# Performance work log

Measured on AMD Instinct MI355X. Metric: run time of the kernel, lower is better.

Reference implementation:

```python
import jax, jax.numpy as jnp
import numpy as np

DN = ('NHWC', 'HWIO', 'NHWC')
EPS = 1e-8
BN_EPS = 1e-3
ROUT_ITERS = 3


def _bn(x, p, axis):
    # p: [4, C] rows = gamma, beta, moving_mean, moving_var (inference-mode BN)
    shp = [1] * x.ndim
    shp[axis % x.ndim] = x.shape[axis % x.ndim]
    g, b, m, v = [p[i].reshape(shp) for i in range(4)]
    return (x - m) * jax.lax.rsqrt(v + BN_EPS) * g + b


def _conv(x, w, b, stride, pad):
    return jax.lax.conv_general_dilated(x, w, (stride, stride), pad, dimension_numbers=DN) + b


def _patches(x, k, s):
    # x: [B, H, W, ...] -> [B, Ho, Wo, k*k, ...] (static k*k strided slices, no big gathers)
    Ho = (x.shape[1] - k) // s + 1
    Wo = (x.shape[2] - k) // s + 1
    sl = [x[:, i:i + s * (Ho - 1) + 1:s, j:j + s * (Wo - 1) + 1:s]
          for i in range(k) for j in range(k)]
    return jnp.stack(sl, axis=3)


def _em_routing(votes, a_in, beta_a, beta_u, iters=ROUT_ITERS):
    # votes: [..., Nin, Nout, D], a_in: [..., Nin]; Hinton matrix-capsule EM routing
    Nout = votes.shape[-2]
    R = jnp.full(votes.shape[:-1], 1.0 / Nout, votes.dtype)  # [..., Nin, Nout]
    a_ex = a_in[..., None]
    for i in range(iters):
        lam = 0.01 * (i + 1)  # inverse-temperature schedule
        Ra = R * a_ex                                             # [..., Nin, Nout]
        Rs = Ra.sum(-2) + EPS                                     # [..., Nout]
        mu = jnp.einsum('...no,...nod->...od', Ra, votes) / Rs[..., None]
        diff2 = (votes - mu[..., None, :, :]) ** 2                # [..., Nin, Nout, D]
        sig2 = jnp.einsum('...no,...nod->...od', Ra, diff2) / Rs[..., None] + EPS
        cost = (beta_u[:, None] + 0.5 * jnp.log(sig2)) * Rs[..., None]
        a_out = jax.nn.sigmoid(lam * (beta_a - cost.sum(-1)))     # [..., Nout]
        if i < iters - 1:
            logp = -0.5 * jnp.sum(diff2 / sig2[..., None, :, :]
                                  + jnp.log(2.0 * jnp.pi * sig2)[..., None, :, :], axis=-1)
            R = jax.nn.softmax(jnp.log(a_out + EPS)[..., None, :] + logp, axis=-1)
    return mu, a_out


def _convcaps(pose, a, W, beta_a, beta_u, k=3, s=2):
    # pose: [B,H,W,C,4,4], a: [B,H,W,C]; W: [k*k*C, Cout, 4, 4]
    pp = _patches(pose, k, s)                  # [B,Ho,Wo,k*k,C,4,4]
    B, Ho, Wo = pp.shape[:3]
    pp = pp.reshape(B, Ho, Wo, -1, 4, 4)       # [B,Ho,Wo,Nin,4,4]
    ap = _patches(a, k, s).reshape(B, Ho, Wo, -1)
    Cout = W.shape[1]
    votes = jnp.einsum('bhwnij,nojk->bhwnoik', pp, W).reshape(B, Ho, Wo, pp.shape[3], Cout, 16)
    mu, a_out = _em_routing(votes, ap, beta_a, beta_u)
    return mu.reshape(B, Ho, Wo, Cout, 4, 4), a_out


def reference(x, conv_w, conv_b, bn1, prim_pose_w, prim_pose_b, prim_act_w, prim_act_b,
              bn2, cc1_w, cc1_ba, cc1_bu, bn3, cc2_w, cc2_ba, cc2_bu, bn4,
              dc_w, dc_ba, dc_bu, dec_w1, dec_b1, dec_w2, dec_b2, dec_w3, dec_b3):
    h = jax.nn.relu(_conv(x, conv_w, conv_b, 2, 'SAME'))          # conv1 + relu
    h = _bn(h, bn1, -1)
    pose = _conv(h, prim_pose_w, prim_pose_b, 2, 'VALID')         # PrimaryCaps pose conv
    B, H, W, _ = pose.shape
    pose = pose.reshape(B, H, W, 32, 4, 4)
    a = jax.nn.sigmoid(_conv(h, prim_act_w, prim_act_b, 2, 'VALID'))
    pose = _bn(pose, bn2, -3)
    pose, a = _convcaps(pose, a, cc1_w, cc1_ba, cc1_bu)
    pose = _bn(pose, bn3, -3)
    pose, a = _convcaps(pose, a, cc2_w, cc2_ba, cc2_bu)
    pose = _bn(pose, bn4, -3)
    # DenseCaps: flatten spatial grid of capsules
    pflat = pose.reshape(B, -1, 4, 4)                             # [B, 1152, 4, 4]
    aflat = a.reshape(B, -1)
    votes = jnp.einsum('bnij,nojk->bnoik', pflat, dc_w).reshape(B, pflat.shape[1], dc_w.shape[1], 16)
    mu, a_out = _em_routing(votes, aflat, dc_ba, dc_bu)           # mu: [B, 32, 16]
    dec_in = mu.reshape(B, -1)                                    # [B, 512]
    h = jax.nn.relu(dec_in @ dec_w1 + dec_b1)
    h = jax.nn.relu(h @ dec_w2 + dec_b2)
    return h @ dec_w3 + dec_b3


def _bn_params(k, C):
    k1, k2, k3, k4 = jax.random.split(k, 4)
    return jnp.stack([1.0 + 0.05 * jax.random.normal(k1, (C,)),
                      0.05 * jax.random.normal(k2, (C,)),
                      0.01 * jax.random.normal(k3, (C,)),
                      1.0 + 0.1 * jax.random.uniform(k4, (C,))]).astype(jnp.float32)


def setup_inputs() -> dict:
    key = jax.random.key(0)
    ks = jax.random.split(key, 24)
    B, HW, NV = 2, 128, 8192
    n = lambda k, s, sc: (sc * jax.random.normal(k, s)).astype(jnp.float32)
    return {
        'x': n(ks[0], (B, HW, HW, 3), 1.0),
        'conv_w': n(ks[1], (11, 11, 3, 96), 0.05), 'conv_b': n(ks[2], (96,), 0.05),
        'bn1': _bn_params(ks[3], 96),
        'prim_pose_w': n(ks[4], (9, 9, 96, 32 * 16), 0.05), 'prim_pose_b': n(ks[5], (32 * 16,), 0.05),
        'prim_act_w': n(ks[6], (9, 9, 96, 32), 0.05), 'prim_act_b': n(ks[7], (32,), 0.05),
        'bn2': _bn_params(ks[8], 32),
        'cc1_w': n(ks[9], (3 * 3 * 32, 32, 4, 4), 0.1),
        'cc1_ba': n(ks[10], (32,), 0.5), 'cc1_bu': n(ks[11], (32,), 0.5),
        'bn3': _bn_params(ks[12], 32),
        'cc2_w': n(ks[13], (3 * 3 * 32, 32, 4, 4), 0.1),
        'cc2_ba': n(ks[14], (32,), 0.5), 'cc2_bu': n(ks[15], (32,), 0.5),
        'bn4': _bn_params(ks[16], 32),
        'dc_w': n(ks[17], (6 * 6 * 32, 32, 4, 4), 0.1),
        'dc_ba': n(ks[18], (32,), 0.5), 'dc_bu': n(ks[19], (32,), 0.5),
        'dec_w1': n(ks[20], (512, 512), 0.05), 'dec_b1': jnp.zeros((512,), jnp.float32),
        'dec_w2': n(ks[21], (512, 1024), 0.05), 'dec_b2': jnp.zeros((1024,), jnp.float32),
        'dec_w3': n(ks[22], (1024, NV), 0.02), 'dec_b3': jnp.zeros((NV,), jnp.float32),
    }
```

## Files before the change

kernel.cpp:

```cpp
#include <hip/hip_runtime.h>
#include <hip/hip_bf16.h>

#define EPSR 1e-8f
#define BNEPS 1e-3f
#define LOG2PI 1.8378770664093453f

typedef _Float16 f16;
typedef _Float16 f16x4 __attribute__((ext_vector_type(4)));
typedef _Float16 f16x8 __attribute__((ext_vector_type(8)));
typedef float f32x4 __attribute__((ext_vector_type(4)));

#define O_H      0
#define O_POSE2  786432
#define O_ACT2   1589248
#define O_POSE3  1639424
#define O_ACT3   1812480
#define O_POSE4  1823296
#define O_ACT4   1860160
#define O_DECIN  1862464
#define O_H1     1863488
#define O_H2     1864512
#define O_PART   1866560
#define O_BWH    1997632
#define O_BWL    4485952
#define NEED_BYTES (6974272ull * 4ull)
#define O_DSTAT  0
#define O_DCOMB  32768

template<int F16>
__global__ __launch_bounds__(256) void conv1_k(
    const float* __restrict__ x, const float* __restrict__ w,
    const float* __restrict__ bias, const float* __restrict__ bn1,
    float* __restrict__ h32, f16* __restrict__ hh, f16* __restrict__ hl)
{
  int t = blockIdx.x * 256 + threadIdx.x;
  int c = t % 96; int px = t / 96;
  int ox = px & 63; int r = px >> 6; int oy = r & 63; int b = r >> 6;
  float acc = 0.f;
  int iy0 = 2*oy - 4, ix0 = 2*ox - 4;
  for (int ky = 0; ky < 11; ++ky) {
    int iy = iy0 + ky;
    if ((unsigned)iy > 127u) continue;
    const float* xrow = x + (size_t)((b*128 + iy)*128)*3;
    const float* wrow = w + (ky*11*3)*96 + c;
    for (int kx = 0; kx < 11; ++kx) {
      int ix = ix0 + kx;
      if ((unsigned)ix > 127u) continue;
      const float* xp = xrow + ix*3;
      const float* wp = wrow + kx*3*96;
      acc = fmaf(xp[0], wp[0],   acc);
      acc = fmaf(xp[1], wp[96],  acc);
      acc = fmaf(xp[2], wp[192], acc);
    }
  }
  acc += bias[c];
  acc = fmaxf(acc, 0.f);
  float g = bn1[c], be = bn1[96+c], mm = bn1[192+c], vv = bn1[288+c];
  float val = (acc - mm) * (g * rsqrtf(vv + BNEPS)) + be;
  if (F16) {
    f16 hi = (f16)val;
    f16 lo = (f16)(val - (float)hi);
    hh[t] = hi; hl[t] = lo;
  } else {
    h32[t] = val;
  }
}

__global__ __launch_bounds__(256) void split_w_k(
    const float* __restrict__ pw, const float* __restrict__ aw,
    f16* __restrict__ bwh, f16* __restrict__ bwl)
{
  __shared__ float tile[32][33];
  const int kb = blockIdx.x * 32, nb = blockIdx.y * 32;
  const int t = threadIdx.x;
  #pragma unroll
  for (int p = 0; p < 4; ++p) {
    int k_l = p*8 + (t>>5), n_l = t & 31;
    int k = kb + k_l, n = nb + n_l;
    float v = 0.f;
    if (n < 512) v = pw[(size_t)k*512 + n];
    else if (n < 544) v = aw[(size_t)k*32 + (n - 512)];
    tile[k_l][n_l] = v;
  }
  __syncthreads();
  #pragma unroll
  for (int p = 0; p < 4; ++p) {
    int n_l = p*8 + (t>>5), k_l = t & 31;
    float v = tile[k_l][n_l];
    f16 hi = (f16)v;
    f16 lo = (f16)(v - (float)hi);
    size_t dst = (size_t)(nb + n_l)*7776 + kb + k_l;
    bwh[dst] = hi; bwl[dst] = lo;
  }
}

__global__ __launch_bounds__(256) void zero_raw(float* __restrict__ pose2, float* __restrict__ act2)
{
  int t = blockIdx.x * 256 + threadIdx.x;
  if (t < 802816) pose2[t] = 0.f;
  else act2[t - 802816] = 0.f;
}

__global__ __launch_bounds__(256, 2) void conv2_mfma(
    const f16* __restrict__ hh, const f16* __restrict__ hl,
    const f16* __restrict__ bwh, const f16* __restrict__ bwl,
    float* __restrict__ pose2r, float* __restrict__ act2r)
{
  __shared__ f16 Ah[128*32];
  __shared__ f16 Al[128*32];
  __shared__ f16 Bh[128*32];
  __shared__ f16 Bl[128*32];
  const int tid = threadIdx.x;
  const int mb = blockIdx.x, nb = blockIdx.y, z = blockIdx.z;
  const int m0 = mb*128, n0 = nb*128;
  const int q = 243 / 8, rch = 243 % 8;
  const int k0 = z*q + (z < rch ? z : rch);
  const int k1 = k0 + q + (z < rch ? 1 : 0);

  const int srow = tid >> 3;
  const int c    = tid & 7;
  int habase[4]; bool amok[4];
  #pragma unroll
  for (int p = 0; p < 4; ++p) {
    int m = m0 + p*32 + srow;
    amok[p] = m < 1568;
    int mm = amok[p] ? m : 0;
    int b = mm / 784; int yx = mm - b*784; int oy = yx / 28, ox = yx - oy*28;
    habase[p] = ((b*64 + 2*oy)*64 + 2*ox)*96;
  }
  size_t bbase[4];
  #pragma unroll
  for (int p = 0; p < 4; ++p) bbase[p] = (size_t)(n0 + p*32 + srow) * 7776;

  f16x4 rah[4], ral[4], rbh[4], rbl[4];
  const f16x4 zv = {(f16)0, (f16)0, (f16)0, (f16)0};

  auto load_step = [&](int kt) {
    int ky = kt / 27, rr = kt % 27; int kx = rr / 3, ci0 = (rr % 3) * 32;
    int aoff = (ky*64 + kx)*96 + ci0 + c*4;
    int koff = kt*32 + c*4;
    #pragma unroll
    for (int p = 0; p < 4; ++p) {
      if (amok[p]) {
        rah[p] = *(const f16x4*)(hh + habase[p] + aoff);
        ral[p] = *(const f16x4*)(hl + habase[p] + aoff);
      } else { rah[p] = zv; ral[p] = zv; }
      rbh[p] = *(const f16x4*)(bwh + bbase[p] + koff);
      rbl[p] = *(const f16x4*)(bwl + bbase[p] + koff);
    }
  };

  int widx[4];
  #pragma unroll
  for (int p = 0; p < 4; ++p) {
    int row = p*32 + srow;
    widx[p] = row*32 + ((((c>>1) + (row>>1)) & 3) << 3) + ((c & 1) << 2);
  }

  const int wv = tid >> 6, lane = tid & 63;
  const int wr = wv >> 1, wc = wv & 1;
  const int l15 = lane & 15, g = lane >> 4;

  f32x4 acc[4][4];
  #pragma unroll
  for (int i = 0; i < 4; ++i)
    #pragma unroll
    for (int j = 0; j < 4; ++j) acc[i][j] = (f32x4){0.f, 0.f, 0.f, 0.f};

  int aidx[4], bidx[4];
  #pragma unroll
  for (int i = 0; i < 4; ++i) {
    int arow = wr*64 + i*16 + l15;
    aidx[i] = arow*32 + (((g + (arow>>1)) & 3) << 3);
    int brow = wc*64 + i*16 + l15;
    bidx[i] = brow*32 + (((g + (brow>>1)) & 3) << 3);
  }

  load_step(k0);
  for (int kt = k0; kt < k1; ++kt) {
    __syncthreads();
    #pragma unroll
    for (int p = 0; p < 4; ++p) {
      *(f16x4*)&Ah[widx[p]] = rah[p];
      *(f16x4*)&Al[widx[p]] = ral[p];
      *(f16x4*)&Bh[widx[p]] = rbh[p];
      *(f16x4*)&Bl[widx[p]] = rbl[p];
    }
    __syncthreads();
    if (kt + 1 < k1) load_step(kt + 1);
    f16x8 ah[4], al[4], bh[4], bl[4];
    #pragma unroll
    for (int i = 0; i < 4; ++i) {
      ah[i] = *(const f16x8*)&Ah[aidx[i]];
      al[i] = *(const f16x8*)&Al[aidx[i]];
      bh[i] = *(const f16x8*)&Bh[bidx[i]];
      bl[i] = *(const f16x8*)&Bl[bidx[i]];
    }
    #pragma unroll
    for (int i = 0; i < 4; ++i)
      #pragma unroll
      for (int j = 0; j < 4; ++j) {
        acc[i][j] = __builtin_amdgcn_mfma_f32_16x16x32_f16(ah[i], bh[j], acc[i][j], 0, 0, 0);
        acc[i][j] = __builtin_amdgcn_mfma_f32_16x16x32_f16(ah[i], bl[j], acc[i][j], 0, 0, 0);
        acc[i][j] = __builtin_amdgcn_mfma_f32_16x16x32_f16(al[i], bh[j], acc[i][j], 0, 0, 0);
      }
  }

  #pragma unroll
  for (int i = 0; i < 4; ++i) {
    #pragma unroll
    for (int j = 0; j < 4; ++j) {
      #pragma unroll
      for (int r2 = 0; r2 < 4; ++r2) {
        int m = m0 + wr*64 + i*16 + g*4 + r2;
        int n = n0 + wc*64 + j*16 + l15;
        if (m < 1568) {
          float val = acc[i][j][r2];
          if (n < 512) atomicAdd(&pose2r[(size_t)m*512 + n], val);
          else if (n < 544) atomicAdd(&act2r[(size_t)m*32 + (n - 512)], val);
        }
      }
    }
  }
}

__global__ __launch_bounds__(256) void conv2_gemm_ks(
    const float* __restrict__ h,
    const float* __restrict__ pw, const float* __restrict__ aw,
    float* __restrict__ pose2r, float* __restrict__ act2r)
{
  __shared__ float As[2][16][68];
  __shared__ float Bs[2][16][68];
  const int tid = threadIdx.x;
  const int mb = blockIdx.x, nb = blockIdx.y, z = blockIdx.z;
  const int m0 = mb * 64;
  const float* Bp; int ldB, n0;
  if (nb < 8) { Bp = pw; ldB = 512; n0 = nb * 64; } else { Bp = aw; ldB = 32; n0 = 0; }

  const int a_ml = tid & 63, a_cig = tid >> 6;
  const int am = m0 + a_ml;
  const bool am_ok = am < 1568;
  int ab_ = am / 784; int ayx = am - ab_*784;
  int aoy = ayx / 28, aox = ayx - aoy*28;
  if (!am_ok) { ab_ = 0; aoy = 0; aox = 0; }
  const float* a_base = h + (size_t)((ab_*64 + 2*aoy)*64 + 2*aox)*96 + a_cig*4;

  const int b_kk = tid >> 4, b_ng = tid & 15;
  const int b_col = b_ng * 4;
  const bool b_ok = b_col < ldB;

  const int tm = (tid & 15) * 4, tn = (tid >> 4) * 4;
  float acc[4][4] = {{0}};

  auto kidx = [](int kt, int& ky, int& kx, int& ci0) {
    int cig = kt % 6; int r = kt / 6; kx = r % 9; ky = r / 9; ci0 = cig * 16;
  };
  auto ldAv = [&](int ky, int kx, int ci0) -> float4 {
    if (!am_ok) return make_float4(0,0,0,0);
    return *(const float4*)(a_base + (ky*64 + kx)*96 + ci0);
  };
  auto ldBv = [&](int kt) -> float4 {
    if (!b_ok) return make_float4(0,0,0,0);
    return *(const float4*)(Bp + (size_t)(kt*16 + b_kk) * ldB + n0 + b_col);
  };
  auto wrAv = [&](float4 v, int buf) {
    As[buf][a_cig*4+0][a_ml] = v.x;
    As[buf][a_cig*4+1][a_ml] = v.y;
    As[buf][a_cig*4+2][a_ml] = v.z;
    As[buf][a_cig*4+3][a_ml] = v.w;
  };
  auto wrBv = [&](float4 v, int buf) {
    *(float4*)&Bs[buf][b_kk][b_col] = v;
  };

  const int kt0 = z * 81;
  {
    int ky, kx, ci0; kidx(kt0, ky, kx, ci0);
    wrAv(ldAv(ky, kx, ci0), 0); wrBv(ldBv(kt0), 0);
  }
  __syncthreads();

  for (int i = 0; i < 81; ++i) {
    int cur = i & 1;
    bool st = i < 80;
    float4 va, vb;
    if (st) {
      int ky, kx, ci0; kidx(kt0 + i + 1, ky, kx, ci0);
      va = ldAv(ky, kx, ci0);
      vb = ldBv(kt0 + i + 1);
    }
    #pragma unroll
    for (int kk = 0; kk < 16; ++kk) {
      float4 av = *(const float4*)&As[cur][kk][tm];
      float4 bv = *(const float4*)&Bs[cur][kk][tn];
      float aa[4] = {av.x, av.y, av.z, av.w};
      float bb4[4] = {bv.x, bv.y, bv.z, bv.w};
      #pragma unroll
      for (int ii = 0; ii < 4; ++ii)
        #pragma unroll
        for (int jj = 0; jj < 4; ++jj)
          acc[ii][jj] = fmaf(aa[ii], bb4[jj], acc[ii][jj]);
    }
    if (st) { wrAv(va, cur ^ 1); wrBv(vb, cur ^ 1); }
    __syncthreads();
  }

  #pragma unroll
  for (int i = 0; i < 4; ++i) {
    int m = m0 + tm + i;
    if (m >= 1568) break;
    #pragma unroll
    for (int j = 0; j < 4; ++j) {
      int nl = tn + j;
      if (nb < 8) {
        atomicAdd(&pose2r[(size_t)m*512 + n0 + nl], acc[i][j]);
      } else if (nl < 32) {
        atomicAdd(&act2r[(size_t)m*32 + nl], acc[i][j]);
      }
    }
  }
}

__global__ __launch_bounds__(256) void conv2_epi(
    const float* __restrict__ pb, const float* __restrict__ ab,
    const float* __restrict__ bn2,
    float* __restrict__ pose2, float* __restrict__ act2)
{
  int t = blockIdx.x * 256 + threadIdx.x;
  if (t < 802816) {
    int n = t & 511;
    float val = pose2[t] + pb[n];
    int caps = n >> 4;
    float g = bn2[caps], be = bn2[32+caps], mm = bn2[64+caps], vv = bn2[96+caps];
    pose2[t] = (val - mm) * (g * rsqrtf(vv + BNEPS)) + be;
  } else {
    int t2 = t - 802816;
    int nl = t2 & 31;
    float val = act2[t2] + ab[nl];
    act2[t2] = 1.f / (1.f + expf(-val));
  }
}

template<int NIN, int NWAVES, bool CONV>
__global__ __launch_bounds__(NWAVES*64) void routing_k(
    const float* __restrict__ pose_in, const float* __restrict__ act_in,
    const float* __restrict__ Wv,
    const float* __restrict__ ba, const float* __restrict__ bu,
    const float* __restrict__ bn,
    float* __restrict__ pose_out, float* __restrict__ act_out,
    int Hin, int Win, int Wout)
{
  constexpr int NT  = NWAVES * 64;
  constexpr int NPW = NIN / NWAVES;
  __shared__ float s1s[NWAVES][32*17];
  __shared__ float s2s[NWAVES][32*17];
  __shared__ float rsP[NWAVES][32];
  __shared__ float muS[32*17], isgS[32*17], lgS[32*17];
  __shared__ float laS[32], lsS[32], aoS[32], RsS[32], S0S[32];

  const int tid = threadIdx.x;
  const int wv = tid >> 6, lane = tid & 63;
  const int o = lane & 31, half = lane >> 5;

  int bb = 0, oy = 0, ox = 0;
  if (CONV) {
    int px = blockIdx.x;
    ox = px % Wout; int t2 = px / Wout; oy = t2 % Wout; bb = t2 / Wout;
  } else {
    bb = blockIdx.x;
  }

  auto ld_n = [&](int n, float4& W0, float4& W1, float4& W2, float4& W3,
                  float4& P0, float4& P1, float& AN) {
    const float* wp = Wv + (size_t)(n*32 + o) * 16;
    W0 = *(const float4*)(wp);
    W1 = *(const float4*)(wp + 4);
    W2 = *(const float4*)(wp + 8);
    W3 = *(const float4*)(wp + 12);
    const float* pp;
    if (CONV) {
      int cc = n & 31, kk = n >> 5;
      int ki = kk / 3, kj = kk - ki*3;
      int pix = (bb*Hin + 2*oy + ki)*Win + 2*ox + kj;
      pp = pose_in + (size_t)(pix*32 + cc) * 16;
      AN = act_in[pix*32 + cc];
    } else {
      pp = pose_in + (size_t)(bb*NIN + n) * 16;
      AN = act_in[bb*NIN + n];
    }
    P0 = *(const float4*)(pp + half*8);
    P1 = *(const float4*)(pp + half*8 + 4);
  };

  float mur[8], isgr[8], lar = 0.f, lsr = 0.f;
  #pragma unroll
  for (int i = 0; i < 8; ++i) { mur[i] = 0.f; isgr[i] = 0.f; }

  for (int p = 0; p < 3; ++p) {
    float lam = 0.01f * (float)(p + 1);
    float s1r[8] = {0,0,0,0,0,0,0,0};
    float s2r[8] = {0,0,0,0,0,0,0,0};
    float rsr = 0.f;

    float4 w0, w1, w2, w3, p0, p1; float an;
    ld_n(wv*NPW, w0, w1, w2, w3, p0, p1, an);

    for (int it = 0; it < NPW; ++it) {
      float4 cw0=w0, cw1=w1, cw2=w2, cw3=w3, cp0=p0, cp1=p1; float can=an;
      if (it + 1 < NPW) ld_n(wv*NPW + it + 1, w0, w1, w2, w3, p0, p1, an);

      float v[8];
      v[0] = fmaf(cp0.x,cw0.x, fmaf(cp0.y,cw1.x, fmaf(cp0.z,cw2.x, cp0.w*cw3.x)));
      v[1] = fmaf(cp0.x,cw0.y, fmaf(cp0.y,cw1.y, fmaf(cp0.z,cw2.y, cp0.w*cw3.y)));
      v[2] = fmaf(cp0.x,cw0.z, fmaf(cp0.y,cw1.z, fmaf(cp0.z,cw2.z, cp0.w*cw3.z)));
      v[3] = fmaf(cp0.x,cw0.w, fmaf(cp0.y,cw1.w, fmaf(cp0.z,cw2.w, cp0.w*cw3.w)));
      v[4] = fmaf(cp1.x,cw0.x, fmaf(cp1.y,cw1.x, fmaf(cp1.z,cw2.x, cp1.w*cw3.x)));
      v[5] = fmaf(cp1.x,cw0.y, fmaf(cp1.y,cw1.y, fmaf(cp1.z,cw2.y, cp1.w*cw3.y)));
      v[6] = fmaf(cp1.x,cw0.z, fmaf(cp1.y,cw1.z, fmaf(cp1.z,cw2.z, cp1.w*cw3.z)));
      v[7] = fmaf(cp1.x,cw0.w, fmaf(cp1.y,cw1.w, fmaf(cp1.z,cw2.w, cp1.w*cw3.w)));

      float R;
      if (p == 0) {
        R = 1.f / 32.f;
      } else {
        float t = 0.f;
        #pragma unroll
        for (int dd = 0; dd < 8; ++dd) { float df = v[dd] - mur[dd]; t = fmaf(df*df, isgr[dd], t); }
        t += __shfl_xor(t, 32, 64);
        float logit = lar - 0.5f * (t + lsr);
        float mx = logit;
        mx = fmaxf(mx, __shfl_xor(mx, 16, 64));
        mx = fmaxf(mx, __shfl_xor(mx,  8, 64));
        mx = fmaxf(mx, __shfl_xor(mx,  4, 64));
        mx = fmaxf(mx, __shfl_xor(mx,  2, 64));
        mx = fmaxf(mx, __shfl_xor(mx,  1, 64));
        float e = expf(logit - mx);
        float se = e;
        se += __shfl_xor(se, 16, 64);
        se += __shfl_xor(se,  8, 64);
        se += __shfl_xor(se,  4, 64);
        se += __shfl_xor(se,  2, 64);
        se += __shfl_xor(se,  1, 64);
        R = e / se;
      }
      float Ra = R * can;
      rsr += Ra;
      #pragma unroll
      for (int dd = 0; dd < 8; ++dd) {
        s1r[dd] = fmaf(Ra, v[dd], s1r[dd]);
        s2r[dd] = fmaf(Ra * v[dd], v[dd], s2r[dd]);
      }
    }

    #pragma unroll
    for (int dd = 0; dd < 8; ++dd) {
      s1s[wv][o*17 + half*8 + dd] = s1r[dd];
      s2s[wv][o*17 + half*8 + dd] = s2r[dd];
    }
    if (!half) rsP[wv][o] = rsr;
    __syncthreads();
    if (tid < 32) {
      float r = 0.f;
      #pragma unroll
      for (int w2 = 0; w2 < NWAVES; ++w2) r += rsP[w2][tid];
      S0S[tid] = r; RsS[tid] = r + EPSR;
    }
    __syncthreads();
    for (int idx = tid; idx < 512; idx += NT) {
      int oo = idx >> 4, d = idx & 15;
      float S1 = 0.f, S2 = 0.f;
      #pragma unroll
      for (int w2 = 0; w2 < NWAVES; ++w2) { S1 += s1s[w2][oo*17+d]; S2 += s2s[w2][oo*17+d]; }
      float Rs = RsS[oo];
      float m_ = S1 / Rs;
      float sg = (S2 - 2.f*m_*S1 + m_*m_*S0S[oo]) / Rs + EPSR;
      muS[oo*17+d]  = m_;
      isgS[oo*17+d] = 1.f / sg;
      lgS[oo*17+d]  = logf(sg);
    }
    __syncthreads();
    if (tid < 32) {
      float L = 0.f;
      #pragma unroll
      for (int d = 0; d < 16; ++d) L += lgS[tid*17 + d];
      float cost = (16.f*bu[tid] + 0.5f*L) * RsS[tid];
      float av = 1.f / (1.f + expf(-lam * (ba[tid] - cost)));
      aoS[tid] = av;
      laS[tid] = logf(av + EPSR);
      lsS[tid] = 16.f*LOG2PI + L;
    }
    __syncthreads();
    if (p < 2) {
      #pragma unroll
      for (int dd = 0; dd < 8; ++dd) {
        mur[dd]  = muS[o*17 + half*8 + dd];
        isgr[dd] = isgS[o*17 + half*8 + dd];
      }
      lar = laS[o]; lsr = lsS[o];
    }
  }

  if (CONV) {
    int pxo = (bb*Wout + oy)*Wout + ox;
    for (int idx = tid; idx < 512; idx += NT) {
      int oo = idx >> 4, d = idx & 15;
      float val = muS[oo*17 + d];
      float g = bn[oo], be = bn[32+oo], mm = bn[64+oo], vv = bn[96+oo];
      val = (val - mm) * (g * rsqrtf(vv + BNEPS)) + be;
      pose_out[(size_t)pxo*512 + idx] = val;
    }
    if (tid < 32) act_out[(size_t)pxo*32 + tid] = aoS[tid];
  } else {
    for (int idx = tid; idx < 512; idx += NT)
      pose_out[(size_t)bb*512 + idx] = muS[(idx>>4)*17 + (idx&15)];
  }
}

template<int P>
__global__ __launch_bounds__(256) void dense_stats(
    const float* __restrict__ pose_in, const float* __restrict__ act_in,
    const float* __restrict__ Wv, const float* __restrict__ comb,
    float* __restrict__ stat)
{
  __shared__ float s1s[4][32*17];
  __shared__ float s2s[4][32*17];
  __shared__ float rsP[4][32];
  const int tid = threadIdx.x;
  const int wv = tid >> 6, lane = tid & 63;
  const int o = lane & 31, half = lane >> 5;
  const int bb = blockIdx.x / 12, chunk = blockIdx.x % 12;

  float mur[8], isgr[8], lar = 0.f, lsr = 0.f;
  if (P > 0) {
    const float* cb = comb + (size_t)bb * 1088;
    #pragma unroll
    for (int dd = 0; dd < 8; ++dd) {
      mur[dd]  = cb[o*16 + half*8 + dd];
      isgr[dd] = cb[512 + o*16 + half*8 + dd];
    }
    lar = cb[1024 + o]; lsr = cb[1056 + o];
  }

  auto ld_n = [&](int n, float4& W0, float4& W1, float4& W2, float4& W3,
                  float4& P0, float4& P1, float& AN) {
    const float* wp = Wv + (size_t)(n*32 + o) * 16;
    W0 = *(const float4*)(wp);
    W1 = *(const float4*)(wp + 4);
    W2 = *(const float4*)(wp + 8);
    W3 = *(const float4*)(wp + 12);
    const float* pp = pose_in + (size_t)(bb*1152 + n) * 16;
    AN = act_in[bb*1152 + n];
    P0 = *(const float4*)(pp + half*8);
    P1 = *(const float4*)(pp + half*8 + 4);
  };

  float s1r[8] = {0,0,0,0,0,0,0,0};
  float s2r[8] = {0,0,0,0,0,0,0,0};
  float rsr = 0.f;

  float4 w0, w1, w2, w3, p0, p1; float an;
  ld_n(chunk*96 + wv*24, w0, w1, w2, w3, p0, p1, an);

  for (int it = 0; it < 24; ++it) {
    float4 cw0=w0, cw1=w1, cw2=w2, cw3=w3, cp0=p0, cp1=p1; float can=an;
    if (it + 1 < 24) ld_n(chunk*96 + wv*24 + it + 1, w0, w1, w2, w3, p0, p1, an);

    float v[8];
    v[0] = fmaf(cp0.x,cw0.x, fmaf(cp0.y,cw1.x, fmaf(cp0.z,cw2.x, cp0.w*cw3.x)));
    v[1] = fmaf(cp0.x,cw0.y, fmaf(cp0.y,cw1.y, fmaf(cp0.z,cw2.y, cp0.w*cw3.y)));
    v[2] = fmaf(cp0.x,cw0.z, fmaf(cp0.y,cw1.z, fmaf(cp0.z,cw2.z, cp0.w*cw3.z)));
    v[3] = fmaf(cp0.x,cw0.w, fmaf(cp0.y,cw1.w, fmaf(cp0.z,cw2.w, cp0.w*cw3.w)));
    v[4] = fmaf(cp1.x,cw0.x, fmaf(cp1.y,cw1.x, fmaf(cp1.z,cw2.x, cp1.w*cw3.x)));
    v[5] = fmaf(cp1.x,cw0.y, fmaf(cp1.y,cw1.y, fmaf(cp1.z,cw2.y, cp1.w*cw3.y)));
    v[6] = fmaf(cp1.x,cw0.z, fmaf(cp1.y,cw1.z, fmaf(cp1.z,cw2.z, cp1.w*cw3.z)));
    v[7] = fmaf(cp1.x,cw0.w, fmaf(cp1.y,cw1.w, fmaf(cp1.z,cw2.w, cp1.w*cw3.w)));

    float R;
    if (P == 0) {
      R = 1.f / 32.f;
    } else {
      float t = 0.f;
      #pragma unroll
      for (int dd = 0; dd < 8; ++dd) { float df = v[dd] - mur[dd]; t = fmaf(df*df, isgr[dd], t); }
      t += __shfl_xor(t, 32, 64);
      float logit = lar - 0.5f * (t + lsr);
      float mx = logit;
      mx = fmaxf(mx, __shfl_xor(mx, 16, 64));
      mx = fmaxf(mx, __shfl_xor(mx,  8, 64));
      mx = fmaxf(mx, __shfl_xor(mx,  4, 64));
      mx = fmaxf(mx, __shfl_xor(mx,  2, 64));
      mx = fmaxf(mx, __shfl_xor(mx,  1, 64));
      float e = expf(logit - mx);
      float se = e;
      se += __shfl_xor(se, 16, 64);
      se += __shfl_xor(se,  8, 64);
      se += __shfl_xor(se,  4, 64);
      se += __shfl_xor(se,  2, 64);
      se += __shfl_xor(se,  1, 64);
      R = e / se;
    }
    float Ra = R * can;
    rsr += Ra;
    #pragma unroll
    for (int dd = 0; dd < 8; ++dd) {
      s1r[dd] = fmaf(Ra, v[dd], s1r[dd]);
      s2r[dd] = fmaf(Ra * v[dd], v[dd], s2r[dd]);
    }
  }

  #pragma unroll
  for (int dd = 0; dd < 8; ++dd) {
    s1s[wv][o*17 + half*8 + dd] = s1r[dd];
    s2s[wv][o*17 + half*8 + dd] = s2r[dd];
  }
  if (!half) rsP[wv][o] = rsr;
  __syncthreads();

  float* out = stat + (size_t)(bb*12 + chunk) * 1056;
  for (int idx = tid; idx < 512; idx += 256) {
    int oo = idx >> 4, d = idx & 15;
    float S1 = 0.f, S2 = 0.f;
    #pragma unroll
    for (int w2 = 0; w2 < 4; ++w2) { S1 += s1s[w2][oo*17+d]; S2 += s2s[w2][oo*17+d]; }
    out[idx] = S1; out[512 + idx] = S2;
  }
  if (tid < 32) {
    float r = 0.f;
    #pragma unroll
    for (int w2 = 0; w2 < 4; ++w2) r += rsP[w2][tid];
    out[1024 + tid] = r;
  }
}

template<int P>
__global__ __launch_bounds__(256) void dense_comb(
    const float* __restrict__ stat,
    const float* __restrict__ ba, const float* __restrict__ bu,
    float* __restrict__ comb, float* __restrict__ decin)
{
  __shared__ float S0S[32], RsS[32], lgS[32*17];
  const int tid = threadIdx.x;
  const int bb = blockIdx.x;
  const float* st = stat + (size_t)bb * 12 * 1056;
  float* cb = comb + (size_t)bb * 1088;

  if (tid < 32) {
    float r = 0.f;
    #pragma unroll
    for (int c = 0; c < 12; ++c) r += st[c*1056 + 1024 + tid];
    S0S[tid] = r; RsS[tid] = r + EPSR;
  }
  __syncthreads();
  for (int idx = tid; idx < 512; idx += 256) {
    int oo = idx >> 4, d = idx & 15;
    float S1 = 0.f, S2 = 0.f;
    #pragma unroll
    for (int c = 0; c < 12; ++c) { S1 += st[c*1056 + idx]; S2 += st[c*1056 + 512 + idx]; }
    float Rs = RsS[oo];
    float m_ = S1 / Rs;
    float sg = (S2 - 2.f*m_*S1 + m_*m_*S0S[oo]) / Rs + EPSR;
    if (P == 2) {
      decin[(size_t)bb*512 + idx] = m_;
    } else {
      cb[idx] = m_;
      cb[512 + idx] = 1.f / sg;
    }
    lgS[oo*17 + d] = logf(sg);
  }
  __syncthreads();
  if (P < 2 && tid < 32) {
    float L = 0.f;
    #pragma unroll
    for (int d = 0; d < 16; ++d) L += lgS[tid*17 + d];
    float lam = 0.01f * (float)(P + 1);
    float cost = (16.f*bu[tid] + 0.5f*L) * RsS[tid];
    float av = 1.f / (1.f + expf(-lam * (ba[tid] - cost)));
    cb[1024 + tid] = logf(av + EPSR);
    cb[1056 + tid] = 16.f*LOG2PI + L;
  }
}

__global__ __launch_bounds__(256) void fc_partial(
    const float* __restrict__ in, const float* __restrict__ W,
    float* __restrict__ part, int K, int N, int CK)
{
  int t = blockIdx.x * 256 + threadIdx.x;
  int nj = N >> 2;
  int j4 = t % nj, ks = t / nj;
  int k0 = ks * CK;
  float4 a0 = make_float4(0,0,0,0), a1 = make_float4(0,0,0,0);
  const float4* Wp = (const float4*)W;
  for (int kk = 0; kk < CK; ++kk) {
    int k = k0 + kk;
    float4 wv = Wp[(size_t)k * nj + j4];
    float f0 = in[k], f1 = in[K + k];
    a0.x = fmaf(f0, wv.x, a0.x); a0.y = fmaf(f0, wv.y, a0.y);
    a0.z = fmaf(f0, wv.z, a0.z); a0.w = fmaf(f0, wv.w, a0.w);
    a1.x = fmaf(f1, wv.x, a1.x); a1.y = fmaf(f1, wv.y, a1.y);
    a1.z = fmaf(f1, wv.z, a1.z); a1.w = fmaf(f1, wv.w, a1.w);
  }
  ((float4*)part)[(size_t)(ks*2 + 0) * nj + j4] = a0;
  ((float4*)part)[(size_t)(ks*2 + 1) * nj + j4] = a1;
}

__global__ __launch_bounds__(256) void fc_reduce(
    const float* __restrict__ part, const float* __restrict__ bias,
    float* __restrict__ out, int N, int KS, int relu)
{
  int t = blockIdx.x * 256 + threadIdx.x;
  int b = t / N, j = t - b*N;
  float s = bias[j];
  for (int ks = 0; ks < KS; ++ks) s += part[(size_t)(ks*2 + b) * N + j];
  if (relu) s = fmaxf(s, 0.f);
  out[(size_t)b*N + j] = s;
}

extern "C" void kernel_launch(void* const* d_in, const int* in_sizes, int n_in,
                              void* d_out, int out_size, void* d_ws, size_t ws_size,
                              hipStream_t stream) {
  const float* x    = (const float*)d_in[0];
  const float* c1w  = (const float*)d_in[1];
  const float* c1b  = (const float*)d_in[2];
  const float* bn1  = (const float*)d_in[3];
  const float* ppw  = (const float*)d_in[4];
  const float* ppb  = (const float*)d_in[5];
  const float* paw  = (const float*)d_in[6];
  const float* pab  = (const float*)d_in[7];
  const float* bn2  = (const float*)d_in[8];
  const float* ccw1 = (const float*)d_in[9];
  const float* cba1 = (const float*)d_in[10];
  const float* cbu1 = (const float*)d_in[11];
  const float* bn3  = (const float*)d_in[12];
  const float* ccw2 = (const float*)d_in[13];
  const float* cba2 = (const float*)d_in[14];
  const float* cbu2 = (const float*)d_in[15];
  const float* bn4  = (const float*)d_in[16];
  const float* dcw  = (const float*)d_in[17];
  const float* dcba = (const float*)d_in[18];
  const float* dcbu = (const float*)d_in[19];
  const float* w1   = (const float*)d_in[20];
  const float* b1   = (const float*)d_in[21];
  const float* w2   = (const float*)d_in[22];
  const float* b2   = (const float*)d_in[23];
  const float* w3   = (const float*)d_in[24];
  const float* b3   = (const float*)d_in[25];

  float* ws    = (float*)d_ws;
  float* h     = ws + O_H;
  f16*   hh    = (f16*)(ws + O_H);
  f16*   hl    = hh + 786432;
  float* pose2 = ws + O_POSE2;
  float* act2  = ws + O_ACT2;
  float* pose3 = ws + O_POSE3;
  float* act3  = ws + O_ACT3;
  float* pose4 = ws + O_POSE4;
  float* act4  = ws + O_ACT4;
  float* decin = ws + O_DECIN;
  float* h1    = ws + O_H1;
  float* h2    = ws + O_H2;
  float* part  = ws + O_PART;
  f16*   bwh   = (f16*)(ws + O_BWH);
  f16*   bwl   = (f16*)(ws + O_BWL);
  float* dstat = ws + O_DSTAT;
  float* dcomb = ws + O_DCOMB;

  const bool fast = ws_size >= NEED_BYTES;

  if (fast) {
    conv1_k<1><<<3072, 256, 0, stream>>>(x, c1w, c1b, bn1, nullptr, hh, hl);
    split_w_k<<<dim3(243, 20), 256, 0, stream>>>(ppw, paw, bwh, bwl);
    zero_raw<<<3332, 256, 0, stream>>>(pose2, act2);
    conv2_mfma<<<dim3(13, 5, 8), 256, 0, stream>>>(hh, hl, bwh, bwl, pose2, act2);
  } else {
    conv1_k<0><<<3072, 256, 0, stream>>>(x, c1w, c1b, bn1, h, nullptr, nullptr);
    zero_raw<<<3332, 256, 0, stream>>>(pose2, act2);
    conv2_gemm_ks<<<dim3(25, 9, 6), 256, 0, stream>>>(h, ppw, paw, pose2, act2);
  }
  conv2_epi<<<3332, 256, 0, stream>>>(ppb, pab, bn2, pose2, act2);
  routing_k<288, 16, true><<<338, 1024, 0, stream>>>(pose2, act2, ccw1, cba1, cbu1, bn3,
                                                     pose3, act3, 28, 28, 13);
  routing_k<288, 16, true><<<72, 1024, 0, stream>>>(pose3, act3, ccw2, cba2, cbu2, bn4,
                                                    pose4, act4, 13, 13, 6);
  dense_stats<0><<<24, 256, 0, stream>>>(pose4, act4, dcw, nullptr, dstat);
  dense_comb<0><<<2, 256, 0, stream>>>(dstat, dcba, dcbu, dcomb, nullptr);
  dense_stats<1><<<24, 256, 0, stream>>>(pose4, act4, dcw, dcomb, dstat);
  dense_comb<1><<<2, 256, 0, stream>>>(dstat, dcba, dcbu, dcomb, nullptr);
  dense_stats<2><<<24, 256, 0, stream>>>(pose4, act4, dcw, dcomb, dstat);
  dense_comb<2><<<2, 256, 0, stream>>>(dstat, dcba, dcbu, dcomb, decin);
  fc_partial<<<16, 256, 0, stream>>>(decin, w1, part, 512, 512, 16);
  fc_reduce<<<4, 256, 0, stream>>>(part, b1, h1, 512, 32, 1);
  fc_partial<<<32, 256, 0, stream>>>(h1, w2, part, 512, 1024, 16);
  fc_reduce<<<8, 256, 0, stream>>>(part, b2, h2, 1024, 32, 1);
  fc_partial<<<256, 256, 0, stream>>>(h2, w3, part, 1024, 8192, 32);
  fc_reduce<<<64, 256, 0, stream>>>(part, b3, (float*)d_out, 8192, 32, 0);
}
```

Measured before the change: 679.5 us.

## Restructure EM routing: per-input-capsule softmax into shared memory, then accumulate stats

The routing and dense-stats kernels are restructured so that each thread owns one input capsule. In a first phase it computes all 32 votes, log-likelihoods and the softmax over outputs, and stores the routing weights in a swizzled shared-memory table. The accumulation phase then reads those weights instead of doing cross-lane shuffle max/sum reductions per vote. The routing block size drops from 1024 to 512 threads. This removes the shuffle-heavy softmax from the inner loop, but votes are now computed twice per iteration, the first phase runs on 288 of 512 threads, and weight loads are uncoalesced and no longer prefetched.

```diff
diff --git a/kernel.cpp b/kernel.cpp
--- a/kernel.cpp
+++ b/kernel.cpp
@@ -341,8 +341,8 @@
   }
 }
 
-template<int NIN, int NWAVES, bool CONV>
-__global__ __launch_bounds__(NWAVES*64) void routing_k(
+template<int NIN>
+__global__ __launch_bounds__(512) void routing2_k(
     const float* __restrict__ pose_in, const float* __restrict__ act_in,
     const float* __restrict__ Wv,
     const float* __restrict__ ba, const float* __restrict__ bu,
@@ -350,11 +350,12 @@
     float* __restrict__ pose_out, float* __restrict__ act_out,
     int Hin, int Win, int Wout)
 {
-  constexpr int NT  = NWAVES * 64;
-  constexpr int NPW = NIN / NWAVES;
-  __shared__ float s1s[NWAVES][32*17];
-  __shared__ float s2s[NWAVES][32*17];
-  __shared__ float rsP[NWAVES][32];
+  constexpr int NW = 8;
+  constexpr int NPW = NIN / NW;
+  __shared__ float RaS[NIN*32];
+  __shared__ float anS[NIN];
+  __shared__ float s1s[NW][32*17];
+  __shared__ float s2s[NW][32*17];
   __shared__ float muS[32*17], isgS[32*17], lgS[32*17];
   __shared__ float laS[32], lsS[32], aoS[32], RsS[32], S0S[32];
 
@@ -362,93 +363,104 @@
   const int wv = tid >> 6, lane = tid & 63;
   const int o = lane & 31, half = lane >> 5;
 
-  int bb = 0, oy = 0, ox = 0;
-  if (CONV) {
-    int px = blockIdx.x;
-    ox = px % Wout; int t2 = px / Wout; oy = t2 % Wout; bb = t2 / Wout;
-  } else {
-    bb = blockIdx.x;
-  }
-
-  auto ld_n = [&](int n, float4& W0, float4& W1, float4& W2, float4& W3,
-                  float4& P0, float4& P1, float& AN) {
-    const float* wp = Wv + (size_t)(n*32 + o) * 16;
-    W0 = *(const float4*)(wp);
-    W1 = *(const float4*)(wp + 4);
-    W2 = *(const float4*)(wp + 8);
-    W3 = *(const float4*)(wp + 12);
-    const float* pp;
-    if (CONV) {
+  int px = blockIdx.x;
+  int ox = px % Wout; int t2 = px / Wout; int oy = t2 % Wout; int bb = t2 / Wout;
+
+  const int na = tid;
+  const bool na_ok = na < NIN;
+  f32x4 pr0, pr1, pr2, pr3; float aa = 0.f;
+  if (na_ok) {
+    int cc = na & 31, kk = na >> 5;
+    int ki = kk / 3, kj = kk - ki*3;
+    int pixa = (bb*Hin + 2*oy + ki)*Win + 2*ox + kj;
+    const float* pp = pose_in + (size_t)(pixa*32 + cc) * 16;
+    pr0 = *(const f32x4*)(pp);
+    pr1 = *(const f32x4*)(pp + 4);
+    pr2 = *(const f32x4*)(pp + 8);
+    pr3 = *(const f32x4*)(pp + 12);
+    aa = act_in[pixa*32 + cc];
+  }
+  const int swzb = na * 32;
+  const int swzx = na & 31;
+
+  for (int p = 0; p < 3; ++p) {
+    float lam = 0.01f * (float)(p + 1);
+
+    if (p == 0) {
+      if (na_ok) {
+        #pragma unroll
+        for (int o2 = 0; o2 < 32; ++o2) RaS[swzb + (o2 ^ swzx)] = 1.f/32.f;
+        anS[na] = aa;
+      }
+    } else {
+      if (na_ok) {
+        const float* wpb = Wv + (size_t)na * 32 * 16;
+        float m = -1e30f;
+        #pragma unroll
+        for (int o2 = 0; o2 < 32; ++o2) {
+          const float* wp = wpb + o2*16;
+          f32x4 w0 = *(const f32x4*)(wp);
+          f32x4 w1 = *(const f32x4*)(wp + 4);
+          f32x4 w2 = *(const f32x4*)(wp + 8);
+          f32x4 w3 = *(const f32x4*)(wp + 12);
+          f32x4 v0 = pr0.x*w0 + pr0.y*w1 + pr0.z*w2 + pr0.w*w3;
+          f32x4 v1 = pr1.x*w0 + pr1.y*w1 + pr1.z*w2 + pr1.w*w3;
+          f32x4 v2 = pr2.x*w0 + pr2.y*w1 + pr2.z*w2 + pr2.w*w3;
+          f32x4 v3 = pr3.x*w0 + pr3.y*w1 + pr3.z*w2 + pr3.w*w3;
+          const float* mo = &muS[o2*17];
+          const float* io = &isgS[o2*17];
+          float t = 0.f;
+          #pragma unroll
+          for (int j = 0; j < 4; ++j) { float df = v0[j]-mo[j];    t = fmaf(df*df, io[j],    t); }
+          #pragma unroll
+          for (int j = 0; j < 4; ++j) { float df = v1[j]-mo[4+j];  t = fmaf(df*df, io[4+j],  t); }
+          #pragma unroll
+          for (int j = 0; j < 4; ++j) { float df = v2[j]-mo[8+j];  t = fmaf(df*df, io[8+j],  t); }
+          #pragma unroll
+          for (int j = 0; j < 4; ++j) { float df = v3[j]-mo[12+j]; t = fmaf(df*df, io[12+j], t); }
+          float l = laS[o2] - 0.5f * (t + lsS[o2]);
+          RaS[swzb + (o2 ^ swzx)] = l;
+          m = fmaxf(m, l);
+        }
+        float se = 0.f;
+        #pragma unroll
+        for (int o2 = 0; o2 < 32; ++o2) {
+          int s = swzb + (o2 ^ swzx);
+          float e = expf(RaS[s] - m);
+          se += e;
+          RaS[s] = e;
+        }
+        anS[na] = aa / se;
+      }
+    }
+    __syncthreads();
+
+    float s1r[8] = {0,0,0,0,0,0,0,0};
+    float s2r[8] = {0,0,0,0,0,0,0,0};
+    float rsr = 0.f;
+    for (int it = 0; it < NPW; ++it) {
+      int n = wv*NPW + it;
+      const float* wp = Wv + (size_t)(n*32 + o) * 16;
+      f32x4 w0 = *(const f32x4*)(wp);
+      f32x4 w1 = *(const f32x4*)(wp + 4);
+      f32x4 w2 = *(const f32x4*)(wp + 8);
+      f32x4 w3 = *(const f32x4*)(wp + 12);
       int cc = n & 31, kk = n >> 5;
       int ki = kk / 3, kj = kk - ki*3;
       int pix = (bb*Hin + 2*oy + ki)*Win + 2*ox + kj;
-      pp = pose_in + (size_t)(pix*32 + cc) * 16;
-      AN = act_in[pix*32 + cc];
-    } else {
-      pp = pose_in + (size_t)(bb*NIN + n) * 16;
-      AN = act_in[bb*NIN + n];
-    }
-    P0 = *(const float4*)(pp + half*8);
-    P1 = *(const float4*)(pp + half*8 + 4);
-  };
-
-  float mur[8], isgr[8], lar = 0.f, lsr = 0.f;
-  #pragma unroll
-  for (int i = 0; i < 8; ++i) { mur[i] = 0.f; isgr[i] = 0.f; }
-
-  for (int p = 0; p < 3; ++p) {
-    float lam = 0.01f * (float)(p + 1);
-    float s1r[8] = {0,0,0,0,0,0,0,0};
-    float s2r[8] = {0,0,0,0,0,0,0,0};
-    float rsr = 0.f;
-
-    float4 w0, w1, w2, w3, p0, p1; float an;
-    ld_n(wv*NPW, w0, w1, w2, w3, p0, p1, an);
-
-    for (int it = 0; it < NPW; ++it) {
-      float4 cw0=w0, cw1=w1, cw2=w2, cw3=w3, cp0=p0, cp1=p1; float can=an;
-      if (it + 1 < NPW) ld_n(wv*NPW + it + 1, w0, w1, w2, w3, p0, p1, an);
-
-      float v[8];
-      v[0] = fmaf(cp0.x,cw0.x, fmaf(cp0.y,cw1.x, fmaf(cp0.z,cw2.x, cp0.w*cw3.x)));
-      v[1] = fmaf(cp0.x,cw0.y, fmaf(cp0.y,cw1.y, fmaf(cp0.z,cw2.y, cp0.w*cw3.y)));
-      v[2] = fmaf(cp0.x,cw0.z, fmaf(cp0.y,cw1.z, fmaf(cp0.z,cw2.z, cp0.w*cw3.z)));
-      v[3] = fmaf(cp0.x,cw0.w, fmaf(cp0.y,cw1.w, fmaf(cp0.z,cw2.w, cp0.w*cw3.w)));
-      v[4] = fmaf(cp1.x,cw0.x, fmaf(cp1.y,cw1.x, fmaf(cp1.z,cw2.x, cp1.w*cw3.x)));
-      v[5] = fmaf(cp1.x,cw0.y, fmaf(cp1.y,cw1.y, fmaf(cp1.z,cw2.y, cp1.w*cw3.y)));
-      v[6] = fmaf(cp1.x,cw0.z, fmaf(cp1.y,cw1.z, fmaf(cp1.z,cw2.z, cp1.w*cw3.z)));
-      v[7] = fmaf(cp1.x,cw0.w, fmaf(cp1.y,cw1.w, fmaf(cp1.z,cw2.w, cp1.w*cw3.w)));
-
-      float R;
-      if (p == 0) {
-        R = 1.f / 32.f;
-      } else {
-        float t = 0.f;
-        #pragma unroll
-        for (int dd = 0; dd < 8; ++dd) { float df = v[dd] - mur[dd]; t = fmaf(df*df, isgr[dd], t); }
-        t += __shfl_xor(t, 32, 64);
-        float logit = lar - 0.5f * (t + lsr);
-        float mx = logit;
-        mx = fmaxf(mx, __shfl_xor(mx, 16, 64));
-        mx = fmaxf(mx, __shfl_xor(mx,  8, 64));
-        mx = fmaxf(mx, __shfl_xor(mx,  4, 64));
-        mx = fmaxf(mx, __shfl_xor(mx,  2, 64));
-        mx = fmaxf(mx, __shfl_xor(mx,  1, 64));
-        float e = expf(logit - mx);
-        float se = e;
-        se += __shfl_xor(se, 16, 64);
-        se += __shfl_xor(se,  8, 64);
-        se += __shfl_xor(se,  4, 64);
-        se += __shfl_xor(se,  2, 64);
-        se += __shfl_xor(se,  1, 64);
-        R = e / se;
-      }
-      float Ra = R * can;
+      const float* pp = pose_in + (size_t)(pix*32 + cc) * 16 + half*8;
+      f32x4 q0 = *(const f32x4*)(pp);
+      f32x4 q1 = *(const f32x4*)(pp + 4);
+      float Ra = RaS[n*32 + (o ^ (n & 31))] * anS[n];
+      f32x4 va = q0.x*w0 + q0.y*w1 + q0.z*w2 + q0.w*w3;
+      f32x4 vb = q1.x*w0 + q1.y*w1 + q1.z*w2 + q1.w*w3;
       rsr += Ra;
       #pragma unroll
-      for (int dd = 0; dd < 8; ++dd) {
-        s1r[dd] = fmaf(Ra, v[dd], s1r[dd]);
-        s2r[dd] = fmaf(Ra * v[dd], v[dd], s2r[dd]);
+      for (int j = 0; j < 4; ++j) {
+        s1r[j]   = fmaf(Ra, va[j], s1r[j]);
+        s1r[4+j] = fmaf(Ra, vb[j], s1r[4+j]);
+        s2r[j]   = fmaf(Ra * va[j], va[j], s2r[j]);
+        s2r[4+j] = fmaf(Ra * vb[j], vb[j], s2r[4+j]);
       }
     }
 
@@ -457,20 +469,20 @@
       s1s[wv][o*17 + half*8 + dd] = s1r[dd];
       s2s[wv][o*17 + half*8 + dd] = s2r[dd];
     }
-    if (!half) rsP[wv][o] = rsr;
+    if (!half) s1s[wv][o*17 + 16] = rsr;
     __syncthreads();
     if (tid < 32) {
       float r = 0.f;
       #pragma unroll
-      for (int w2 = 0; w2 < NWAVES; ++w2) r += rsP[w2][tid];
+      for (int w2 = 0; w2 < NW; ++w2) r += s1s[w2][tid*17 + 16];
       S0S[tid] = r; RsS[tid] = r + EPSR;
     }
     __syncthreads();
-    for (int idx = tid; idx < 512; idx += NT) {
-      int oo = idx >> 4, d = idx & 15;
+    {
+      int oo = tid >> 4, d = tid & 15;
       float S1 = 0.f, S2 = 0.f;
       #pragma unroll
-      for (int w2 = 0; w2 < NWAVES; ++w2) { S1 += s1s[w2][oo*17+d]; S2 += s2s[w2][oo*17+d]; }
+      for (int w2 = 0; w2 < NW; ++w2) { S1 += s1s[w2][oo*17+d]; S2 += s2s[w2][oo*17+d]; }
       float Rs = RsS[oo];
       float m_ = S1 / Rs;
       float sg = (S2 - 2.f*m_*S1 + m_*m_*S0S[oo]) / Rs + EPSR;
@@ -490,121 +502,118 @@
       lsS[tid] = 16.f*LOG2PI + L;
     }
     __syncthreads();
-    if (p < 2) {
-      #pragma unroll
-      for (int dd = 0; dd < 8; ++dd) {
-        mur[dd]  = muS[o*17 + half*8 + dd];
-        isgr[dd] = isgS[o*17 + half*8 + dd];
-      }
-      lar = laS[o]; lsr = lsS[o];
-    }
-  }
-
-  if (CONV) {
-    int pxo = (bb*Wout + oy)*Wout + ox;
-    for (int idx = tid; idx < 512; idx += NT) {
-      int oo = idx >> 4, d = idx & 15;
-      float val = muS[oo*17 + d];
-      float g = bn[oo], be = bn[32+oo], mm = bn[64+oo], vv = bn[96+oo];
-      val = (val - mm) * (g * rsqrtf(vv + BNEPS)) + be;
-      pose_out[(size_t)pxo*512 + idx] = val;
-    }
-    if (tid < 32) act_out[(size_t)pxo*32 + tid] = aoS[tid];
-  } else {
-    for (int idx = tid; idx < 512; idx += NT)
-      pose_out[(size_t)bb*512 + idx] = muS[(idx>>4)*17 + (idx&15)];
-  }
+  }
+
+  int pxo = (bb*Wout + oy)*Wout + ox;
+  {
+    int oo = tid >> 4, d = tid & 15;
+    float val = muS[oo*17 + d];
+    float g = bn[oo], be = bn[32+oo], mm = bn[64+oo], vv = bn[96+oo];
+    val = (val - mm) * (g * rsqrtf(vv + BNEPS)) + be;
+    pose_out[(size_t)pxo*512 + tid] = val;
+  }
+  if (tid < 32) act_out[(size_t)pxo*32 + tid] = aoS[tid];
 }
 
 template<int P>
-__global__ __launch_bounds__(256) void dense_stats(
+__global__ __launch_bounds__(256) void dense_stats2(
     const float* __restrict__ pose_in, const float* __restrict__ act_in,
     const float* __restrict__ Wv, const float* __restrict__ comb,
     float* __restrict__ stat)
 {
-  __shared__ float s1s[4][32*17];
-  __shared__ float s2s[4][32*17];
-  __shared__ float rsP[4][32];
+  constexpr int NW = 4;
+  __shared__ float RaS[96*32];
+  __shared__ float anS[96];
+  __shared__ float s1s[NW][32*17];
+  __shared__ float s2s[NW][32*17];
   const int tid = threadIdx.x;
   const int wv = tid >> 6, lane = tid & 63;
   const int o = lane & 31, half = lane >> 5;
   const int bb = blockIdx.x / 12, chunk = blockIdx.x % 12;
-
-  float mur[8], isgr[8], lar = 0.f, lsr = 0.f;
-  if (P > 0) {
-    const float* cb = comb + (size_t)bb * 1088;
-    #pragma unroll
-    for (int dd = 0; dd < 8; ++dd) {
-      mur[dd]  = cb[o*16 + half*8 + dd];
-      isgr[dd] = cb[512 + o*16 + half*8 + dd];
-    }
-    lar = cb[1024 + o]; lsr = cb[1056 + o];
-  }
-
-  auto ld_n = [&](int n, float4& W0, float4& W1, float4& W2, float4& W3,
-                  float4& P0, float4& P1, float& AN) {
-    const float* wp = Wv + (size_t)(n*32 + o) * 16;
-    W0 = *(const float4*)(wp);
-    W1 = *(const float4*)(wp + 4);
-    W2 = *(const float4*)(wp + 8);
-    W3 = *(const float4*)(wp + 12);
-    const float* pp = pose_in + (size_t)(bb*1152 + n) * 16;
-    AN = act_in[bb*1152 + n];
-    P0 = *(const float4*)(pp + half*8);
-    P1 = *(const float4*)(pp + half*8 + 4);
-  };
+  const int n0 = chunk * 96;
+
+  if (P == 0) {
+    if (tid < 96) {
+      int n = n0 + tid;
+      float aa = act_in[bb*1152 + n];
+      #pragma unroll
+      for (int o2 = 0; o2 < 32; ++o2) RaS[tid*32 + (o2 ^ (tid & 31))] = 1.f/32.f;
+      anS[tid] = aa;
+    }
+  } else {
+    if (tid < 96) {
+      int n = n0 + tid;
+      const float* pp = pose_in + (size_t)(bb*1152 + n) * 16;
+      f32x4 pr0 = *(const f32x4*)(pp);
+      f32x4 pr1 = *(const f32x4*)(pp + 4);
+      f32x4 pr2 = *(const f32x4*)(pp + 8);
+      f32x4 pr3 = *(const f32x4*)(pp + 12);
+      float aa = act_in[bb*1152 + n];
+      const float* cb = comb + (size_t)bb * 1088;
+      const float* wpb = Wv + (size_t)n * 32 * 16;
+      const int swzb = tid*32, swzx = tid & 31;
+      float m = -1e30f;
+      for (int o2 = 0; o2 < 32; ++o2) {
+        const float* wp = wpb + o2*16;
+        f32x4 w0 = *(const f32x4*)(wp);
+        f32x4 w1 = *(const f32x4*)(wp + 4);
+        f32x4 w2 = *(const f32x4*)(wp + 8);
+        f32x4 w3 = *(const f32x4*)(wp + 12);
+        f32x4 v0 = pr0.x*w0 + pr0.y*w1 + pr0.z*w2 + pr0.w*w3;
+        f32x4 v1 = pr1.x*w0 + pr1.y*w1 + pr1.z*w2 + pr1.w*w3;
+        f32x4 v2 = pr2.x*w0 + pr2.y*w1 + pr2.z*w2 + pr2.w*w3;
+        f32x4 v3 = pr3.x*w0 + pr3.y*w1 + pr3.z*w2 + pr3.w*w3;
+        const float* mo = cb + o2*16;
+        const float* io = cb + 512 + o2*16;
+        float t = 0.f;
+        #pragma unroll
+        for (int j = 0; j < 4; ++j) { float df = v0[j]-mo[j];    t = fmaf(df*df, io[j],    t); }
+        #pragma unroll
+        for (int j = 0; j < 4; ++j) { float df = v1[j]-mo[4+j];  t = fmaf(df*df, io[4+j],  t); }
+        #pragma unroll
+        for (int j = 0; j < 4; ++j) { float df = v2[j]-mo[8+j];  t = fmaf(df*df, io[8+j],  t); }
+        #pragma unroll
+        for (int j = 0; j < 4; ++j) { float df = v3[j]-mo[12+j]; t = fmaf(df*df, io[12+j], t); }
+        float l = cb[1024 + o2] - 0.5f * (t + cb[1056 + o2]);
+        RaS[swzb + (o2 ^ swzx)] = l;
+        m = fmaxf(m, l);
+      }
+      float se = 0.f;
+      for (int o2 = 0; o2 < 32; ++o2) {
+        int s = swzb + (o2 ^ swzx);
+        float e = expf(RaS[s] - m);
+        se += e;
+        RaS[s] = e;
+      }
+      anS[tid] = aa / se;
+    }
+  }
+  __syncthreads();
 
   float s1r[8] = {0,0,0,0,0,0,0,0};
   float s2r[8] = {0,0,0,0,0,0,0,0};
   float rsr = 0.f;
-
-  float4 w0, w1, w2, w3, p0, p1; float an;
-  ld_n(chunk*96 + wv*24, w0, w1, w2, w3, p0, p1, an);
-
   for (int it = 0; it < 24; ++it) {
-    float4 cw0=w0, cw1=w1, cw2=w2, cw3=w3, cp0=p0, cp1=p1; float can=an;
-    if (it + 1 < 24) ld_n(chunk*96 + wv*24 + it + 1, w0, w1, w2, w3, p0, p1, an);
-
-    float v[8];
-    v[0] = fmaf(cp0.x,cw0.x, fmaf(cp0.y,cw1.x, fmaf(cp0.z,cw2.x, cp0.w*cw3.x)));
-    v[1] = fmaf(cp0.x,cw0.y, fmaf(cp0.y,cw1.y, fmaf(cp0.z,cw2.y, cp0.w*cw3.y)));
-    v[2] = fmaf(cp0.x,cw0.z, fmaf(cp0.y,cw1.z, fmaf(cp0.z,cw2.z, cp0.w*cw3.z)));
-    v[3] = fmaf(cp0.x,cw0.w, fmaf(cp0.y,cw1.w, fmaf(cp0.z,cw2.w, cp0.w*cw3.w)));
-    v[4] = fmaf(cp1.x,cw0.x, fmaf(cp1.y,cw1.x, fmaf(cp1.z,cw2.x, cp1.w*cw3.x)));
-    v[5] = fmaf(cp1.x,cw0.y, fmaf(cp1.y,cw1.y, fmaf(cp1.z,cw2.y, cp1.w*cw3.y)));
-    v[6] = fmaf(cp1.x,cw0.z, fmaf(cp1.y,cw1.z, fmaf(cp1.z,cw2.z, cp1.w*cw3.z)));
-    v[7] = fmaf(cp1.x,cw0.w, fmaf(cp1.y,cw1.w, fmaf(cp1.z,cw2.w, cp1.w*cw3.w)));
-
-    float R;
-    if (P == 0) {
-      R = 1.f / 32.f;
-    } else {
-      float t = 0.f;
-      #pragma unroll
-      for (int dd = 0; dd < 8; ++dd) { float df = v[dd] - mur[dd]; t = fmaf(df*df, isgr[dd], t); }
-      t += __shfl_xor(t, 32, 64);
-      float logit = lar - 0.5f * (t + lsr);
-      float mx = logit;
-      mx = fmaxf(mx, __shfl_xor(mx, 16, 64));
-      mx = fmaxf(mx, __shfl_xor(mx,  8, 64));
-      mx = fmaxf(mx, __shfl_xor(mx,  4, 64));
-      mx = fmaxf(mx, __shfl_xor(mx,  2, 64));
-      mx = fmaxf(mx, __shfl_xor(mx,  1, 64));
-      float e = expf(logit - mx);
-      float se = e;
-      se += __shfl_xor(se, 16, 64);
-      se += __shfl_xor(se,  8, 64);
-      se += __shfl_xor(se,  4, 64);
-      se += __shfl_xor(se,  2, 64);
-      se += __shfl_xor(se,  1, 64);
-      R = e / se;
-    }
-    float Ra = R * can;
+    int nl = wv*24 + it;
+    int n = n0 + nl;
+    const float* wp = Wv + (size_t)(n*32 + o) * 16;
+    f32x4 w0 = *(const f32x4*)(wp);
+    f32x4 w1 = *(const f32x4*)(wp + 4);
+    f32x4 w2 = *(const f32x4*)(wp + 8);
+    f32x4 w3 = *(const f32x4*)(wp + 12);
+    const float* pp = pose_in + (size_t)(bb*1152 + n) * 16 + half*8;
+    f32x4 q0 = *(const f32x4*)(pp);
+    f32x4 q1 = *(const f32x4*)(pp + 4);
+    float Ra = RaS[nl*32 + (o ^ (nl & 31))] * anS[nl];
+    f32x4 va = q0.x*w0 + q0.y*w1 + q0.z*w2 + q0.w*w3;
+    f32x4 vb = q1.x*w0 + q1.y*w1 + q1.z*w2 + q1.w*w3;
     rsr += Ra;
     #pragma unroll
-    for (int dd = 0; dd < 8; ++dd) {
-      s1r[dd] = fmaf(Ra, v[dd], s1r[dd]);
-      s2r[dd] = fmaf(Ra * v[dd], v[dd], s2r[dd]);
+    for (int j = 0; j < 4; ++j) {
+      s1r[j]   = fmaf(Ra, va[j], s1r[j]);
+      s2r[j]   = fmaf(Ra * va[j], va[j], s2r[j]);
+      s1r[4+j] = fmaf(Ra, vb[j], s1r[4+j]);
+      s2r[4+j] = fmaf(Ra * vb[j], vb[j], s2r[4+j]);
     }
   }
 
@@ -613,7 +622,7 @@
     s1s[wv][o*17 + half*8 + dd] = s1r[dd];
     s2s[wv][o*17 + half*8 + dd] = s2r[dd];
   }
-  if (!half) rsP[wv][o] = rsr;
+  if (!half) s1s[wv][o*17 + 16] = rsr;
   __syncthreads();
 
   float* out = stat + (size_t)(bb*12 + chunk) * 1056;
@@ -621,13 +630,13 @@
     int oo = idx >> 4, d = idx & 15;
     float S1 = 0.f, S2 = 0.f;
     #pragma unroll
-    for (int w2 = 0; w2 < 4; ++w2) { S1 += s1s[w2][oo*17+d]; S2 += s2s[w2][oo*17+d]; }
+    for (int w2 = 0; w2 < NW; ++w2) { S1 += s1s[w2][oo*17+d]; S2 += s2s[w2][oo*17+d]; }
     out[idx] = S1; out[512 + idx] = S2;
   }
   if (tid < 32) {
     float r = 0.f;
     #pragma unroll
-    for (int w2 = 0; w2 < 4; ++w2) r += rsP[w2][tid];
+    for (int w2 = 0; w2 < NW; ++w2) r += s1s[w2][tid*17 + 16];
     out[1024 + tid] = r;
   }
 }
@@ -777,15 +786,15 @@
     conv2_gemm_ks<<<dim3(25, 9, 6), 256, 0, stream>>>(h, ppw, paw, pose2, act2);
   }
   conv2_epi<<<3332, 256, 0, stream>>>(ppb, pab, bn2, pose2, act2);
-  routing_k<288, 16, true><<<338, 1024, 0, stream>>>(pose2, act2, ccw1, cba1, cbu1, bn3,
-                                                     pose3, act3, 28, 28, 13);
-  routing_k<288, 16, true><<<72, 1024, 0, stream>>>(pose3, act3, ccw2, cba2, cbu2, bn4,
-                                                    pose4, act4, 13, 13, 6);
-  dense_stats<0><<<24, 256, 0, stream>>>(pose4, act4, dcw, nullptr, dstat);
+  routing2_k<288><<<338, 512, 0, stream>>>(pose2, act2, ccw1, cba1, cbu1, bn3,
+                                           pose3, act3, 28, 28, 13);
+  routing2_k<288><<<72, 512, 0, stream>>>(pose3, act3, ccw2, cba2, cbu2, bn4,
+                                          pose4, act4, 13, 13, 6);
+  dense_stats2<0><<<24, 256, 0, stream>>>(pose4, act4, dcw, nullptr, dstat);
   dense_comb<0><<<2, 256, 0, stream>>>(dstat, dcba, dcbu, dcomb, nullptr);
-  dense_stats<1><<<24, 256, 0, stream>>>(pose4, act4, dcw, dcomb, dstat);
+  dense_stats2<1><<<24, 256, 0, stream>>>(pose4, act4, dcw, dcomb, dstat);
   dense_comb<1><<<2, 256, 0, stream>>>(dstat, dcba, dcbu, dcomb, nullptr);
-  dense_stats<2><<<24, 256, 0, stream>>>(pose4, act4, dcw, dcomb, dstat);
+  dense_stats2<2><<<24, 256, 0, stream>>>(pose4, act4, dcw, dcomb, dstat);
   dense_comb<2><<<2, 256, 0, stream>>>(dstat, dcba, dcbu, dcomb, decin);
   fc_partial<<<16, 256, 0, stream>>>(decin, w1, part, 512, 512, 16);
   fc_reduce<<<4, 256, 0, stream>>>(part, b1, h1, 512, 32, 1);
```

After: 804.6 us. 18.4% more time.
